# Performance work log

Hardware: AMD Instinct MI355X
Metric: run time of the kernel (lower is better)

The kernel has to match this reference:

```python
import jax, jax.numpy as jnp
import numpy as np

PAD_IDX = 0
NEG = -1e9


def gru_step(h, x, Wih, Whh, bih, bhh):
    # PyTorch GRU cell. Wih: [3H, In], Whh: [3H, H]
    gi = x @ Wih.T + bih
    gh = h @ Whh.T + bhh
    H = h.shape[-1]
    i_r, i_z, i_n = gi[..., :H], gi[..., H:2 * H], gi[..., 2 * H:]
    h_r, h_z, h_n = gh[..., :H], gh[..., H:2 * H], gh[..., 2 * H:]
    r = jax.nn.sigmoid(i_r + h_r)
    z = jax.nn.sigmoid(i_z + h_z)
    n = jnp.tanh(i_n + r * h_n)
    return (1.0 - z) * n + z * h


def setup_inputs() -> dict:
    key = jax.random.key(0)
    V, E, H, C = 256, 512, 1024, 128
    NM, NT, NP = 8, 12, 8
    B, S, T = 256, 96, 40
    ks = iter(jax.random.split(key, 40))

    def p(shape, scale=0.05):
        return (jax.random.normal(next(ks), shape, dtype=jnp.float32) * scale)

    enc_emb = p((V, E)).at[PAD_IDX].set(0.0)
    dec_emb = p((V, E)).at[PAD_IDX].set(0.0)
    inp = dict(
        src=jax.random.randint(next(ks), (B, S), 0, V, dtype=jnp.int32),
        tgt=jax.random.randint(next(ks), (B, T), 0, V, dtype=jnp.int32),
        mode_idx=jax.random.randint(next(ks), (B,), 0, NM, dtype=jnp.int32),
        tense_idx=jax.random.randint(next(ks), (B,), 0, NT, dtype=jnp.int32),
        person_idx=jax.random.randint(next(ks), (B,), 0, NP, dtype=jnp.int32),
        enc_emb=enc_emb,
        enc_Wih_f=p((3 * H, E)), enc_Whh_f=p((3 * H, H)),
        enc_bih_f=p((3 * H,)), enc_bhh_f=p((3 * H,)),
        enc_Wih_b=p((3 * H, E)), enc_Whh_b=p((3 * H, H)),
        enc_bih_b=p((3 * H,)), enc_bhh_b=p((3 * H,)),
        Wa=p((H, 3 * H)),           # attn: Linear(2H + H -> H), no bias
        va=p((1, H)),               # v: Linear(H -> 1), no bias
        dec_emb=dec_emb,
        dec_Wih=p((3 * H, E + 2 * H)), dec_Whh=p((3 * H, H)),
        dec_bih=p((3 * H,)), dec_bhh=p((3 * H,)),
        Wfc=p((V, H + 2 * H + E)), bfc=p((V,)),
        mode_E=p((NM, C)).at[0].set(0.0),
        tense_E=p((NT, C)).at[0].set(0.0),
        person_E=p((NP, C)).at[0].set(0.0),
        Wbr=p((H, 2 * H + 3 * C)), bbr=p((H,)),
    )
    return inp


def reference(src, tgt, mode_idx, tense_idx, person_idx,
              enc_emb, enc_Wih_f, enc_Whh_f, enc_bih_f, enc_bhh_f,
              enc_Wih_b, enc_Whh_b, enc_bih_b, enc_bhh_b,
              Wa, va, dec_emb, dec_Wih, dec_Whh, dec_bih, dec_bhh,
              Wfc, bfc, mode_E, tense_E, person_E, Wbr, bbr):
    B, S = src.shape
    T = tgt.shape[1]
    H = dec_Whh.shape[1]

    # ---- Encoder: bidirectional GRU ----
    x = enc_emb[src]                       # [B,S,E]
    xs = jnp.swapaxes(x, 0, 1)             # [S,B,E]
    h0 = jnp.zeros((B, H), dtype=x.dtype)

    def fstep(h, xt):
        h2 = gru_step(h, xt, enc_Wih_f, enc_Whh_f, enc_bih_f, enc_bhh_f)
        return h2, h2

    def bstep(h, xt):
        h2 = gru_step(h, xt, enc_Wih_b, enc_Whh_b, enc_bih_b, enc_bhh_b)
        return h2, h2

    hf, outs_f = jax.lax.scan(fstep, h0, xs)
    hb, outs_b = jax.lax.scan(bstep, h0, xs[::-1])
    outs_b = outs_b[::-1]
    enc_out = jnp.swapaxes(jnp.concatenate([outs_f, outs_b], axis=-1), 0, 1)  # [B,S,2H]
    enc_hidden = jnp.concatenate([hf, hb], axis=-1)                           # [B,2H]

    # ---- Bridge init of decoder hidden ----
    cond = jnp.concatenate([enc_hidden, mode_E[mode_idx], tense_E[tense_idx],
                            person_E[person_idx]], axis=-1)
    dec_h0 = jnp.tanh(cond @ Wbr.T + bbr)  # [B,H]

    # ---- Attention precompute (linear is separable over the concat) ----
    Wa_h, Wa_e = Wa[:, :H], Wa[:, H:]
    enc_proj = jnp.einsum('bsd,hd->bsh', enc_out, Wa_e)  # [B,S,H]
    src_mask = (src != PAD_IDX)

    # ---- Decoder greedy loop (eval: no teacher forcing) ----
    def step(carry, _):
        h, tok = carry
        energy = jnp.tanh(h @ Wa_h.T[None] if False else jnp.tanh(0))  # placeholder
        energy = jnp.tanh((h @ Wa_h.T)[:, None, :] + enc_proj)          # [B,S,H]
        scores = jnp.einsum('bsh,h->bs', energy, va[0])
        scores = jnp.where(src_mask, scores, NEG)
        w = jax.nn.softmax(scores, axis=-1)
        ctx = jnp.einsum('bs,bsd->bd', w, enc_out)                      # [B,2H]
        emb = dec_emb[tok]                                              # [B,E]
        rnn_in = jnp.concatenate([emb, ctx], axis=-1)
        h2 = gru_step(h, rnn_in, dec_Wih, dec_Whh, dec_bih, dec_bhh)
        pred = jnp.concatenate([h2, ctx, emb], axis=-1) @ Wfc.T + bfc   # [B,V]
        tok2 = jnp.argmax(pred, axis=-1).astype(tok.dtype)
        return (h2, tok2), pred

    (_, _), preds = jax.lax.scan(step, (dec_h0, tgt[:, 0]), None, length=T - 1)
    return jnp.swapaxes(preds, 0, 1)  # [B, T-1, V]
```

## Files before the change

kernel.cpp:

```cpp
#include <hip/hip_runtime.h>
#include <hip/hip_fp16.h>
#include <cstdint>
#include <cstddef>

#define B_  256
#define S_  96
#define T_  40
#define V_  256
#define E_  512
#define H_  1024
#define C_  128

typedef __attribute__((ext_vector_type(8))) short s8v;
typedef __attribute__((ext_vector_type(4))) float f4v;

__device__ __forceinline__ float sigmoidf_(float x) { return 1.0f / (1.0f + expf(-x)); }

__device__ __forceinline__ uint32_t cvtpk_bf16(float a, float b) {
  uint32_t r;
  asm("v_cvt_pk_bf16_f32 %0, %1, %2" : "=v"(r) : "v"(a), "v"(b));
  return r;
}

union U4 { uint32_t u[4]; s8v v; };

__device__ __forceinline__ void split8(const float4 a, const float4 b, s8v& hi, s8v& lo) {
  U4 H, L;
  H.u[0] = cvtpk_bf16(a.x, a.y);
  H.u[1] = cvtpk_bf16(a.z, a.w);
  H.u[2] = cvtpk_bf16(b.x, b.y);
  H.u[3] = cvtpk_bf16(b.z, b.w);
  const float r0 = a.x - __uint_as_float(H.u[0] << 16);
  const float r1 = a.y - __uint_as_float(H.u[0] & 0xffff0000u);
  const float r2 = a.z - __uint_as_float(H.u[1] << 16);
  const float r3 = a.w - __uint_as_float(H.u[1] & 0xffff0000u);
  const float r4 = b.x - __uint_as_float(H.u[2] << 16);
  const float r5 = b.y - __uint_as_float(H.u[2] & 0xffff0000u);
  const float r6 = b.z - __uint_as_float(H.u[3] << 16);
  const float r7 = b.w - __uint_as_float(H.u[3] & 0xffff0000u);
  L.u[0] = cvtpk_bf16(r0, r1);
  L.u[1] = cvtpk_bf16(r2, r3);
  L.u[2] = cvtpk_bf16(r4, r5);
  L.u[3] = cvtpk_bf16(r6, r7);
  hi = H.v; lo = L.v;
}

__global__ void wsplit_k(const float* __restrict__ Wf, const float* __restrict__ Wb,
                         short* __restrict__ hi, short* __restrict__ lo, int n)
{
  const int i = blockIdx.x * 256 + threadIdx.x;
  const float w = (i < n) ? Wf[i] : Wb[i - n];
  const uint32_t h = cvtpk_bf16(w, w) & 0xffffu;
  const float wh = __uint_as_float(h << 16);
  const uint32_t l = cvtpk_bf16(w - wh, w - wh) & 0xffffu;
  hi[i] = (short)h;
  lo[i] = (short)l;
}

__global__ void split_plane_k(const float* __restrict__ src, int ld_src, int col0,
                              short* __restrict__ hi, short* __restrict__ lo,
                              int ld_p, int pcol0, int total, int cols)
{
  const int i = blockIdx.x * 256 + threadIdx.x;
  if (i >= total) return;
  const int r = i / cols, c = i % cols;
  const float w = src[(size_t)r * ld_src + col0 + c];
  const uint32_t h = cvtpk_bf16(w, w) & 0xffffu;
  const float wh = __uint_as_float(h << 16);
  const uint32_t l = cvtpk_bf16(w - wh, w - wh) & 0xffffu;
  const size_t o = (size_t)r * ld_p + pcol0 + c;
  hi[o] = (short)h;
  lo[o] = (short)l;
}

struct EM {
  const int* gidx; int goff0, goff1;
  const float* Gt0; const float* Gt1;
  const float* h0; const float* h1; int ldh;
  const short* whi; const short* wlo;
  const float* bih0; const float* bih1;
  const float* bhh0; const float* bhh1;
  float* d0; float* d1;
  __half* e0; __half* e1; int lde;
};

__global__ __launch_bounds__(256)
void enc_mfma_k(EM g)
{
  const int fid = (blockIdx.x & 7) * 64 + (blockIdx.x >> 3);
  const int m0 = (fid & 3) * 64;
  const int r2 = fid >> 2;
  const int dir = r2 & 1;
  const int q0 = (r2 >> 1) * 16;

  __shared__ int rows[64];
  const int tid = threadIdx.x;
  if (tid < 64)
    rows[tid] = g.gidx[(size_t)(m0 + tid) * S_ + (dir ? g.goff1 : g.goff0)];
  __syncthreads();

  const int w = tid >> 6, lane = tid & 63;
  const int arow = m0 + 16 * w + (lane & 15);
  const int kc = (lane >> 4) << 3;
  const float* hsrc = dir ? g.h1 : g.h0;
  const short* whi = g.whi + (size_t)dir * (3u * H_ * H_);
  const short* wlo = g.wlo + (size_t)dir * (3u * H_ * H_);
  const float* ap = hsrc + (size_t)arow * g.ldh;
  const int wrow = q0 + (lane & 15);

  f4v acc[3];
  acc[0] = f4v{0.f, 0.f, 0.f, 0.f};
  acc[1] = f4v{0.f, 0.f, 0.f, 0.f};
  acc[2] = f4v{0.f, 0.f, 0.f, 0.f};

  float4 a0 = *(const float4*)(ap + kc);
  float4 a1 = *(const float4*)(ap + kc + 4);
  s8v bh[3], bl[3];
#pragma unroll
  for (int g3 = 0; g3 < 3; ++g3) {
    const size_t wb = (size_t)(g3 * H_ + wrow) * H_ + kc;
    bh[g3] = *(const s8v*)(whi + wb);
    bl[g3] = *(const s8v*)(wlo + wb);
  }

  for (int kb = 0; kb < 1024; kb += 32) {
    float4 na0, na1;
    s8v nbh[3], nbl[3];
    if (kb + 32 < 1024) {
      na0 = *(const float4*)(ap + kb + 32 + kc);
      na1 = *(const float4*)(ap + kb + 32 + kc + 4);
#pragma unroll
      for (int g3 = 0; g3 < 3; ++g3) {
        const size_t wb = (size_t)(g3 * H_ + wrow) * H_ + kb + 32 + kc;
        nbh[g3] = *(const s8v*)(whi + wb);
        nbl[g3] = *(const s8v*)(wlo + wb);
      }
    }
    s8v ah, al;
    split8(a0, a1, ah, al);
#pragma unroll
    for (int g3 = 0; g3 < 3; ++g3) {
      acc[g3] = __builtin_amdgcn_mfma_f32_16x16x32_bf16(ah, bh[g3], acc[g3], 0, 0, 0);
      acc[g3] = __builtin_amdgcn_mfma_f32_16x16x32_bf16(al, bh[g3], acc[g3], 0, 0, 0);
      acc[g3] = __builtin_amdgcn_mfma_f32_16x16x32_bf16(ah, bl[g3], acc[g3], 0, 0, 0);
    }
    a0 = na0; a1 = na1;
#pragma unroll
    for (int g3 = 0; g3 < 3; ++g3) { bh[g3] = nbh[g3]; bl[g3] = nbl[g3]; }
  }

  const float* bih = dir ? g.bih1 : g.bih0;
  const float* bhh = dir ? g.bhh1 : g.bhh0;
  const float* Gt = dir ? g.Gt1 : g.Gt0;
  float* dst = dir ? g.d1 : g.d0;
  __half* edst = dir ? g.e1 : g.e0;
  const int col = q0 + (lane & 15);
  const float bir = bih[col], biz = bih[H_ + col], bin = bih[2 * H_ + col];
  const float bhr = bhh[col], bhz = bhh[H_ + col], bhn = bhh[2 * H_ + col];
#pragma unroll
  for (int r = 0; r < 4; ++r) {
    const int b = m0 + 16 * w + (lane >> 4) * 4 + r;
    const float* Gr = Gt + (size_t)rows[b - m0] * (3 * H_);
    const float hold = hsrc[(size_t)b * g.ldh + col];
    const float rr = sigmoidf_(acc[0][r] + Gr[col] + bir + bhr);
    const float zz = sigmoidf_(acc[1][r] + Gr[H_ + col] + biz + bhz);
    const float nn = tanhf(Gr[2 * H_ + col] + bin + rr * (acc[2][r] + bhn));
    const float hv = (1.f - zz) * nn + zz * hold;
    dst[(size_t)b * H_ + col] = hv;
    edst[(size_t)b * g.lde + col] = __float2half(hv);
  }
}

struct DM {
  const float* predin;
  const float* h;
  const int* tok;
  const float* Gd;
  const short* whi; const short* wlo;
  const float* bih; const float* bhh;
  float* d;
  float* predout;
};

__global__ __launch_bounds__(256)
void dec_mfma_k(DM g)
{
  const int fid = (blockIdx.x & 7) * 32 + (blockIdx.x >> 3);
  const int m0 = (fid & 3) * 64;
  const int q0 = (fid >> 2) * 16;
  const int tid = threadIdx.x;
  const int w = tid >> 6, lane = tid & 63;
  const int arow = m0 + 16 * w + (lane & 15);
  const int kc = (lane >> 4) << 3;
  const float* actx = g.predin + (size_t)arow * 3584 + 1024;
  const float* ahid = g.h + (size_t)arow * H_;
  const int wrow = q0 + (lane & 15);

  f4v aR = f4v{0.f,0.f,0.f,0.f}, aZ = aR, aNI = aR, aNH = aR;

  auto loadA = [&](int kk, float4& x0, float4& x1) {
    const float* p = (kk < 2048) ? (actx + kk) : (ahid + kk - 2048);
    x0 = *(const float4*)p;
    x1 = *(const float4*)(p + 4);
  };

  float4 a0, a1;
  loadA(kc, a0, a1);
  s8v bh[3], bl[3];
#pragma unroll
  for (int g3 = 0; g3 < 3; ++g3) {
    const size_t wb = (size_t)(g3 * H_ + wrow) * 3072 + kc;
    bh[g3] = *(const s8v*)(g.whi + wb);
    bl[g3] = *(const s8v*)(g.wlo + wb);
  }

  for (int kb = 0; kb < 3072; kb += 32) {
    float4 na0, na1;
    s8v nbh[3], nbl[3];
    if (kb + 32 < 3072) {
      loadA(kb + 32 + kc, na0, na1);
#pragma unroll
      for (int g3 = 0; g3 < 3; ++g3) {
        const size_t wb = (size_t)(g3 * H_ + wrow) * 3072 + kb + 32 + kc;
        nbh[g3] = *(const s8v*)(g.whi + wb);
        nbl[g3] = *(const s8v*)(g.wlo + wb);
      }
    }
    s8v ah, al;
    split8(a0, a1, ah, al);
    aR = __builtin_amdgcn_mfma_f32_16x16x32_bf16(ah, bh[0], aR, 0, 0, 0);
    aR = __builtin_amdgcn_mfma_f32_16x16x32_bf16(al, bh[0], aR, 0, 0, 0);
    aR = __builtin_amdgcn_mfma_f32_16x16x32_bf16(ah, bl[0], aR, 0, 0, 0);
    aZ = __builtin_amdgcn_mfma_f32_16x16x32_bf16(ah, bh[1], aZ, 0, 0, 0);
    aZ = __builtin_amdgcn_mfma_f32_16x16x32_bf16(al, bh[1], aZ, 0, 0, 0);
    aZ = __builtin_amdgcn_mfma_f32_16x16x32_bf16(ah, bl[1], aZ, 0, 0, 0);
    if (kb < 2048) {
      aNI = __builtin_amdgcn_mfma_f32_16x16x32_bf16(ah, bh[2], aNI, 0, 0, 0);
      aNI = __builtin_amdgcn_mfma_f32_16x16x32_bf16(al, bh[2], aNI, 0, 0, 0);
      aNI = __builtin_amdgcn_mfma_f32_16x16x32_bf16(ah, bl[2], aNI, 0, 0, 0);
    } else {
      aNH = __builtin_amdgcn_mfma_f32_16x16x32_bf16(ah, bh[2], aNH, 0, 0, 0);
      aNH = __builtin_amdgcn_mfma_f32_16x16x32_bf16(al, bh[2], aNH, 0, 0, 0);
      aNH = __builtin_amdgcn_mfma_f32_16x16x32_bf16(ah, bl[2], aNH, 0, 0, 0);
    }
    a0 = na0; a1 = na1;
#pragma unroll
    for (int g3 = 0; g3 < 3; ++g3) { bh[g3] = nbh[g3]; bl[g3] = nbl[g3]; }
  }

  const int col = q0 + (lane & 15);
  const float bir = g.bih[col], biz = g.bih[H_ + col], bin = g.bih[2 * H_ + col];
  const float bhr = g.bhh[col], bhz = g.bhh[H_ + col], bhn = g.bhh[2 * H_ + col];
#pragma unroll
  for (int r = 0; r < 4; ++r) {
    const int b = m0 + 16 * w + (lane >> 4) * 4 + r;
    const float* Gr = g.Gd + (size_t)g.tok[b] * (3 * H_);
    const float hold = g.h[(size_t)b * H_ + col];
    const float rr = sigmoidf_(aR[r] + Gr[col] + bir + bhr);
    const float zz = sigmoidf_(aZ[r] + Gr[H_ + col] + biz + bhz);
    const float nn = tanhf(aNI[r] + Gr[2 * H_ + col] + bin + rr * (aNH[r] + bhn));
    const float hv = (1.f - zz) * nn + zz * hold;
    g.d[(size_t)b * H_ + col] = hv;
    g.predout[(size_t)b * 3584 + col] = hv;
  }
}

__global__ __launch_bounds__(256)
void prqa_mfma_k(const float* __restrict__ predin,
                 const short* __restrict__ fhi, const short* __restrict__ flo,
                 const float* __restrict__ bfc,
                 const float* __restrict__ hnew,
                 const short* __restrict__ qhi, const short* __restrict__ qlo,
                 float* __restrict__ out_t, float* __restrict__ qout)
{
  const int bid = blockIdx.x, tid = threadIdx.x;
  const int w = tid >> 6, lane = tid & 63;
  const int kc = (lane >> 4) << 3;
  if (bid < 256) {
    const int m0 = (bid >> 4) << 4, n0 = (bid & 15) << 4;
    const float* ap = predin + (size_t)(m0 + (lane & 15)) * 3584 + w * 896;
    const short* bhp = fhi + (size_t)(n0 + (lane & 15)) * 3584 + w * 896;
    const short* blp = flo + (size_t)(n0 + (lane & 15)) * 3584 + w * 896;
    f4v acc = f4v{0.f, 0.f, 0.f, 0.f};
    float4 a0 = *(const float4*)(ap + kc), a1 = *(const float4*)(ap + kc + 4);
    s8v bh = *(const s8v*)(bhp + kc), bl = *(const s8v*)(blp + kc);
    for (int kb = 0; kb < 896; kb += 32) {
      float4 na0, na1; s8v nbh, nbl;
      if (kb + 32 < 896) {
        na0 = *(const float4*)(ap + kb + 32 + kc);
        na1 = *(const float4*)(ap + kb + 32 + kc + 4);
        nbh = *(const s8v*)(bhp + kb + 32 + kc);
        nbl = *(const s8v*)(blp + kb + 32 + kc);
      }
      s8v ah, al;
      split8(a0, a1, ah, al);
      acc = __builtin_amdgcn_mfma_f32_16x16x32_bf16(ah, bh, acc, 0, 0, 0);
      acc = __builtin_amdgcn_mfma_f32_16x16x32_bf16(al, bh, acc, 0, 0, 0);
      acc = __builtin_amdgcn_mfma_f32_16x16x32_bf16(ah, bl, acc, 0, 0, 0);
      a0 = na0; a1 = na1; bh = nbh; bl = nbl;
    }
    __shared__ float red[4][64][4];
#pragma unroll
    for (int r = 0; r < 4; ++r) red[w][lane][r] = acc[r];
    __syncthreads();
    const int row = tid >> 4, col = tid & 15;
    const int sl = col + ((row >> 2) << 4), reg = row & 3;
    const float s = red[0][sl][reg] + red[1][sl][reg] + red[2][sl][reg] + red[3][sl][reg];
    out_t[(size_t)(m0 + row) * ((T_ - 1) * V_) + n0 + col] = s + bfc[n0 + col];
  } else {
    const int tt = (bid - 256) * 4 + w;
    const int m0 = (tt >> 6) << 4, n0 = (tt & 63) << 4;
    const float* ap = hnew + (size_t)(m0 + (lane & 15)) * H_;
    const short* bhp = qhi + (size_t)(n0 + (lane & 15)) * H_;
    const short* blp = qlo + (size_t)(n0 + (lane & 15)) * H_;
    f4v acc = f4v{0.f, 0.f, 0.f, 0.f};
    float4 a0 = *(const float4*)(ap + kc), a1 = *(const float4*)(ap + kc + 4);
    s8v bh = *(const s8v*)(bhp + kc), bl = *(const s8v*)(blp + kc);
    for (int kb = 0; kb < 1024; kb += 32) {
      float4 na0, na1; s8v nbh, nbl;
      if (kb + 32 < 1024) {
        na0 = *(const float4*)(ap + kb + 32 + kc);
        na1 = *(const float4*)(ap + kb + 32 + kc + 4);
        nbh = *(const s8v*)(bhp + kb + 32 + kc);
        nbl = *(const s8v*)(blp + kb + 32 + kc);
      }
      s8v ah, al;
      split8(a0, a1, ah, al);
      acc = __builtin_amdgcn_mfma_f32_16x16x32_bf16(ah, bh, acc, 0, 0, 0);
      acc = __builtin_amdgcn_mfma_f32_16x16x32_bf16(al, bh, acc, 0, 0, 0);
      acc = __builtin_amdgcn_mfma_f32_16x16x32_bf16(ah, bl, acc, 0, 0, 0);
      a0 = na0; a1 = na1; bh = nbh; bl = nbl;
    }
#pragma unroll
    for (int r = 0; r < 4; ++r)
      qout[(size_t)(m0 + (lane >> 4) * 4 + r) * H_ + n0 + (lane & 15)] = acc[r];
  }
}

__global__ __launch_bounds__(512)
void attn1_k(const float* __restrict__ out, const int* __restrict__ tgt,
             const float* __restrict__ q, const __half* __restrict__ proj,
             const float* __restrict__ va, const int* __restrict__ src,
             const float* __restrict__ dec_emb,
             float* __restrict__ predin, float* __restrict__ wts,
             int* __restrict__ tokbuf, int t)
{
  const int b = blockIdx.x, tid = threadIdx.x;
  const int lane = tid & 63, wv = tid >> 6;
  __shared__ float sm[128];
  __shared__ float tr[128];
  __shared__ float rv[4];
  __shared__ int ri[4];
  __shared__ int tok_s;
  if (t == 0) {
    if (tid == 0) tok_s = tgt[(size_t)b * T_];
  } else {
    if (tid < 256) {
      float av = out[((size_t)b * (T_ - 1) + (t - 1)) * V_ + tid];
      int ai = tid;
      for (int off = 32; off; off >>= 1) {
        const float ov = __shfl_down(av, off);
        const int   oi = __shfl_down(ai, off);
        if (ov > av) { av = ov; ai = oi; }
      }
      if (lane == 0) { rv[wv] = av; ri[wv] = ai; }
    }
    __syncthreads();
    if (tid == 0) {
      float bv = rv[0]; int bi = ri[0];
      for (int w2 = 1; w2 < 4; ++w2) if (rv[w2] > bv) { bv = rv[w2]; bi = ri[w2]; }
      tok_s = bi;
    }
  }
  __syncthreads();
  const int tok = tok_s;
  if (tid == 0) tokbuf[b] = tok;
  predin[(size_t)b * 3584 + 3072 + tid] = dec_emb[(size_t)tok * E_ + tid];
  const float* qb = q + (size_t)b * H_;
  for (int s = wv * 12; s < wv * 12 + 12; ++s) {
    const __half* pb = proj + ((size_t)b * S_ + s) * H_;
    float part = 0.f;
#pragma unroll
    for (int j = 0; j < 8; ++j) {
      const int h = lane * 2 + j * 128;
      const __half2 p2 = *(const __half2*)(pb + h);
      const float2 q2 = *(const float2*)(qb + h);
      const float2 v2 = *(const float2*)(va + h);
      part += v2.x * tanhf(q2.x + __half2float(p2.x));
      part += v2.y * tanhf(q2.y + __half2float(p2.y));
    }
    for (int off = 32; off; off >>= 1) part += __shfl_down(part, off);
    if (lane == 0)
      sm[s] = (src[(size_t)b * S_ + s] == 0) ? -1.0e9f : part;
  }
  __syncthreads();
  if (tid < 128) tr[tid] = (tid < S_) ? sm[tid] : -3.0e38f;
  __syncthreads();
  for (int s2 = 64; s2 > 0; s2 >>= 1) { if (tid < s2) tr[tid] = fmaxf(tr[tid], tr[tid + s2]); __syncthreads(); }
  const float mx = tr[0];
  __syncthreads();
  if (tid < 128) tr[tid] = (tid < S_) ? expf(sm[tid] - mx) : 0.f;
  __syncthreads();
  for (int s2 = 64; s2 > 0; s2 >>= 1) { if (tid < s2) tr[tid] += tr[tid + s2]; __syncthreads(); }
  const float inv = 1.0f / tr[0];
  __syncthreads();
  if (tid < S_) wts[(size_t)b * S_ + tid] = expf(sm[tid] - mx) * inv;
}

__global__ __launch_bounds__(256)
void ctx_k(const float* __restrict__ wts, const __half* __restrict__ enc,
           float* __restrict__ predin)
{
  const int b = blockIdx.y, tid = threadIdx.x;
  __shared__ float sw[S_];
  if (tid < S_) sw[tid] = wts[(size_t)b * S_ + tid];
  __syncthreads();
  const int d = blockIdx.x * 512 + tid * 2;
  const __half* eb = enc + (size_t)b * S_ * (2 * H_) + d;
  float c0 = 0.f, c1 = 0.f;
  for (int s0 = 0; s0 < S_; s0 += 8) {
    __half2 v[8];
#pragma unroll
    for (int i = 0; i < 8; ++i) v[i] = *(const __half2*)(eb + (size_t)(s0 + i) * (2 * H_));
#pragma unroll
    for (int i = 0; i < 8; ++i) {
      const float w = sw[s0 + i];
      c0 += w * __half2float(v[i].x);
      c1 += w * __half2float(v[i].y);
    }
  }
  *(float2*)(predin + (size_t)b * 3584 + H_ + d) = make_float2(c0, c1);
}

struct GB {
  const float* A; int lda;
  const __half* Ah;
  const float* W; int ldw;
  const float* bias;
  float* C; int ldc;
  __half* Ch;
  int M, N, K, act;
  const float *hf, *hb; int ldh;
  const float *mE, *tE, *pE;
  const int *mi, *ti, *pi;
};

template<int AMODE, int CMODE>
__global__ __launch_bounds__(256)
void gemm_k(GB g0, GB g1)
{
  GB g = blockIdx.z ? g1 : g0;
  const int m0 = blockIdx.y * 64, n0 = blockIdx.x * 64;
  if (m0 >= g.M || n0 >= g.N) return;
  __shared__ float As[32][68];
  __shared__ float Ws[32][68];
  const int tid = threadIdx.x, tx = tid & 15, ty = tid >> 4;
  const int lm = tid >> 3, lk = (tid & 7) << 2;
  float acc[4][4] = {};
  float4 av[2], wv[2], av2[2], wv2[2];

  auto load_tile = [&](int k0, float4 (&AV)[2], float4 (&WV)[2]) {
#pragma unroll
    for (int i = 0; i < 2; ++i) {
      const int row = lm + i * 32;
      const int kk = k0 + lk;
      if (AMODE == 0) {
        AV[i] = *(const float4*)(g.A + (size_t)(m0 + row) * g.lda + kk);
      } else if (AMODE == 4) {
        const __half* ap = g.Ah + (size_t)(m0 + row) * g.lda + kk;
        const __half2 h0 = *(const __half2*)ap;
        const __half2 h1 = *(const __half2*)(ap + 2);
        AV[i] = make_float4(__half2float(h0.x), __half2float(h0.y),
                            __half2float(h1.x), __half2float(h1.y));
      } else {
        const int mg = m0 + row; const float* sp; size_t o;
        if (kk < 1024)      { sp = g.hf; o = (size_t)mg * g.ldh + kk; }
        else if (kk < 2048) { sp = g.hb; o = (size_t)mg * g.ldh + kk - 1024; }
        else if (kk < 2176) { sp = g.mE; o = (size_t)g.mi[mg] * C_ + kk - 2048; }
        else if (kk < 2304) { sp = g.tE; o = (size_t)g.ti[mg] * C_ + kk - 2176; }
        else                { sp = g.pE; o = (size_t)g.pi[mg] * C_ + kk - 2304; }
        AV[i] = *(const float4*)(sp + o);
      }
      WV[i] = *(const float4*)(g.W + (size_t)(n0 + row) * g.ldw + kk);
    }
  };

  load_tile(0, av, wv);
  for (int k0 = 0; k0 < g.K; k0 += 32) {
    __syncthreads();
#pragma unroll
    for (int i = 0; i < 2; ++i) {
      const int row = lm + i * 32;
      As[lk + 0][row] = av[i].x; As[lk + 1][row] = av[i].y;
      As[lk + 2][row] = av[i].z; As[lk + 3][row] = av[i].w;
      Ws[lk + 0][row] = wv[i].x; Ws[lk + 1][row] = wv[i].y;
      Ws[lk + 2][row] = wv[i].z; Ws[lk + 3][row] = wv[i].w;
    }
    __syncthreads();
    if (k0 + 32 < g.K) load_tile(k0 + 32, av2, wv2);
#pragma unroll
    for (int k = 0; k < 32; ++k) {
      const float4 a4 = *(const float4*)&As[k][ty << 2];
      const float4 b4 = *(const float4*)&Ws[k][tx << 2];
      acc[0][0] += a4.x * b4.x; acc[0][1] += a4.x * b4.y; acc[0][2] += a4.x * b4.z; acc[0][3] += a4.x * b4.w;
      acc[1][0] += a4.y * b4.x; acc[1][1] += a4.y * b4.y; acc[1][2] += a4.y * b4.z; acc[1][3] += a4.y * b4.w;
      acc[2][0] += a4.z * b4.x; acc[2][1] += a4.z * b4.y; acc[2][2] += a4.z * b4.z; acc[2][3] += a4.z * b4.w;
      acc[3][0] += a4.w * b4.x; acc[3][1] += a4.w * b4.y; acc[3][2] += a4.w * b4.z; acc[3][3] += a4.w * b4.w;
    }
#pragma unroll
    for (int i = 0; i < 2; ++i) { av[i] = av2[i]; wv[i] = wv2[i]; }
  }
  const int n = n0 + (tx << 2);
  float4 bb = make_float4(0.f, 0.f, 0.f, 0.f);
  if (g.bias) bb = *(const float4*)(g.bias + n);
#pragma unroll
  for (int i = 0; i < 4; ++i) {
    const int m = m0 + (ty << 2) + i;
    float4 v = make_float4(acc[i][0] + bb.x, acc[i][1] + bb.y, acc[i][2] + bb.z, acc[i][3] + bb.w);
    if (CMODE == 0) {
      if (g.act) { v.x = tanhf(v.x); v.y = tanhf(v.y); v.z = tanhf(v.z); v.w = tanhf(v.w); }
      *(float4*)(g.C + (size_t)m * g.ldc + n) = v;
    } else {
      __half2* cp = (__half2*)(g.Ch + (size_t)m * g.ldc + n);
      cp[0] = __floats2half2_rn(v.x, v.y);
      cp[1] = __floats2half2_rn(v.z, v.w);
    }
  }
}

__global__ void zero_k(float* __restrict__ p, int n)
{
  const int i = blockIdx.x * 256 + threadIdx.x;
  if (i < n) p[i] = 0.0f;
}

__global__ void sentinel_k(float* out, float v) { out[threadIdx.x] = v; }

extern "C" void kernel_launch(void* const* d_in, const int* in_sizes, int n_in,
                              void* d_out, int out_size, void* d_ws, size_t ws_size,
                              hipStream_t stream)
{
  const int*   src        = (const int*)d_in[0];
  const int*   tgt        = (const int*)d_in[1];
  const int*   mode_idx   = (const int*)d_in[2];
  const int*   tense_idx  = (const int*)d_in[3];
  const int*   person_idx = (const int*)d_in[4];
  const float* enc_emb    = (const float*)d_in[5];
  const float* eWih_f     = (const float*)d_in[6];
  const float* eWhh_f     = (const float*)d_in[7];
  const float* ebih_f     = (const float*)d_in[8];
  const float* ebhh_f     = (const float*)d_in[9];
  const float* eWih_b     = (const float*)d_in[10];
  const float* eWhh_b     = (const float*)d_in[11];
  const float* ebih_b     = (const float*)d_in[12];
  const float* ebhh_b     = (const float*)d_in[13];
  const float* Wa         = (const float*)d_in[14];
  const float* va         = (const float*)d_in[15];
  const float* dec_emb    = (const float*)d_in[16];
  const float* dWih       = (const float*)d_in[17];
  const float* dWhh       = (const float*)d_in[18];
  const float* dbih       = (const float*)d_in[19];
  const float* dbhh       = (const float*)d_in[20];
  const float* Wfc        = (const float*)d_in[21];
  const float* bfc        = (const float*)d_in[22];
  const float* mode_E     = (const float*)d_in[23];
  const float* tense_E    = (const float*)d_in[24];
  const float* person_E   = (const float*)d_in[25];
  const float* Wbr        = (const float*)d_in[26];
  const float* bbr        = (const float*)d_in[27];
  float* out = (float*)d_out;

  char* base = (char*)d_ws;
  size_t off = 0;
  auto alloc = [&](size_t bytes) { char* r = base + off; off = (off + bytes + 255) & ~(size_t)255; return r; };
  __half* enc_out = (__half*)alloc(2ull * B_ * S_ * 2 * H_);
  __half* proj    = (__half*)alloc(2ull * B_ * S_ * H_);
  short* whh_hi = (short*)alloc(2ull * 2 * 3 * H_ * H_);
  short* whh_lo = (short*)alloc(2ull * 2 * 3 * H_ * H_);
  short* dpl_hi = (short*)alloc(2ull * 3 * H_ * 3072);
  short* dpl_lo = (short*)alloc(2ull * 3 * H_ * 3072);
  short* fc_hi  = (short*)alloc(2ull * V_ * 3584);
  short* fc_lo  = (short*)alloc(2ull * V_ * 3584);
  short* qa_hi  = (short*)alloc(2ull * H_ * H_);
  short* qa_lo  = (short*)alloc(2ull * H_ * H_);
  float* Gi_f  = (float*)alloc(4ull * V_ * 3 * H_);
  float* Gi_b  = (float*)alloc(4ull * V_ * 3 * H_);
  float* Gd    = (float*)alloc(4ull * V_ * 3 * H_);
  float* hfA   = (float*)alloc(4ull * B_ * H_);
  float* hfB   = (float*)alloc(4ull * B_ * H_);
  float* hbA   = (float*)alloc(4ull * B_ * H_);
  float* hbB   = (float*)alloc(4ull * B_ * H_);
  float* h_d0  = (float*)alloc(4ull * B_ * H_);
  float* h_d1  = (float*)alloc(4ull * B_ * H_);
  float* q     = (float*)alloc(4ull * B_ * H_);
  float* predin = (float*)alloc(4ull * B_ * 3584);
  float* wts   = (float*)alloc(4ull * B_ * S_);
  int*   tok   = (int*)alloc(4ull * B_);
  float* zero_buf = (float*)alloc(4ull * 1024);
  if (off > ws_size) {
    hipLaunchKernelGGL(sentinel_k, dim3(1), dim3(256), 0, stream, out,
                       1000.0f + (float)(ws_size >> 20));
    return;
  }

  hipLaunchKernelGGL(zero_k, dim3(4), dim3(256), 0, stream, zero_buf, 1024);

  {
    const int n = 3 * H_ * H_;
    hipLaunchKernelGGL(wsplit_k, dim3((2 * n) / 256), dim3(256), 0, stream,
                       eWhh_f, eWhh_b, whh_hi, whh_lo, n);
    int tot = 3 * H_ * 2048;
    hipLaunchKernelGGL(split_plane_k, dim3((tot + 255) / 256), dim3(256), 0, stream,
                       dWih, 2560, 512, dpl_hi, dpl_lo, 3072, 0, tot, 2048);
    tot = 3 * H_ * 1024;
    hipLaunchKernelGGL(split_plane_k, dim3((tot + 255) / 256), dim3(256), 0, stream,
                       dWhh, 1024, 0, dpl_hi, dpl_lo, 3072, 2048, tot, 1024);
    tot = V_ * 3584;
    hipLaunchKernelGGL(split_plane_k, dim3((tot + 255) / 256), dim3(256), 0, stream,
                       Wfc, 3584, 0, fc_hi, fc_lo, 3584, 0, tot, 3584);
    tot = H_ * 1024;
    hipLaunchKernelGGL(split_plane_k, dim3((tot + 255) / 256), dim3(256), 0, stream,
                       Wa, 3 * H_, 0, qa_hi, qa_lo, 1024, 0, tot, 1024);
  }

  GB Z{};

  {
    GB t0 = Z, t1 = Z;
    t0.A = enc_emb; t0.lda = E_; t0.W = eWih_f; t0.ldw = E_;
    t0.C = Gi_f; t0.ldc = 3 * H_; t0.M = V_; t0.N = 3 * H_; t0.K = E_;
    t1 = t0; t1.W = eWih_b; t1.C = Gi_b;
    hipLaunchKernelGGL((gemm_k<0, 0>), dim3(48, 4, 2), dim3(256), 0, stream, t0, t1);
    GB t2 = Z;
    t2.A = dec_emb; t2.lda = E_; t2.W = dWih; t2.ldw = 2560;
    t2.C = Gd; t2.ldc = 3 * H_; t2.M = V_; t2.N = 3 * H_; t2.K = E_;
    hipLaunchKernelGGL((gemm_k<0, 0>), dim3(48, 4, 1), dim3(256), 0, stream, t2, t2);
  }

  for (int t = 0; t < S_; ++t) {
    EM em{};
    em.gidx = src; em.goff0 = t; em.goff1 = S_ - 1 - t;
    em.Gt0 = Gi_f; em.Gt1 = Gi_b;
    if (t == 0) { em.h0 = zero_buf; em.h1 = zero_buf; em.ldh = 0; }
    else if (t & 1) { em.h0 = hfA; em.h1 = hbA; em.ldh = H_; }
    else            { em.h0 = hfB; em.h1 = hbB; em.ldh = H_; }
    em.whi = whh_hi; em.wlo = whh_lo;
    em.bih0 = ebih_f; em.bih1 = ebih_b; em.bhh0 = ebhh_f; em.bhh1 = ebhh_b;
    if (t & 1) { em.d0 = hfB; em.d1 = hbB; } else { em.d0 = hfA; em.d1 = hbA; }
    em.e0 = enc_out + (size_t)t * 2 * H_;
    em.e1 = enc_out + (size_t)(S_ - 1 - t) * 2 * H_ + H_;
    em.lde = S_ * 2 * H_;
    hipLaunchKernelGGL(enc_mfma_k, dim3(512), dim3(256), 0, stream, em);
  }
  float* hf_fin = hfB;
  float* hb_fin = hbB;

  {
    GB ep = Z;
    ep.Ah = enc_out; ep.lda = 2 * H_; ep.W = Wa + H_; ep.ldw = 3 * H_;
    ep.Ch = proj; ep.ldc = H_; ep.M = B_ * S_; ep.N = H_; ep.K = 2 * H_;
    hipLaunchKernelGGL((gemm_k<4, 1>), dim3(16, 384, 1), dim3(256), 0, stream, ep, ep);
  }

  {
    GB br = Z;
    br.W = Wbr; br.ldw = 2432; br.bias = bbr; br.C = h_d0; br.ldc = H_;
    br.M = B_; br.N = H_; br.K = 2432; br.act = 1;
    br.hf = hf_fin; br.hb = hb_fin; br.ldh = H_;
    br.mE = mode_E; br.tE = tense_E; br.pE = person_E;
    br.mi = mode_idx; br.ti = tense_idx; br.pi = person_idx;
    hipLaunchKernelGGL((gemm_k<2, 0>), dim3(16, 4, 1), dim3(256), 0, stream, br, br);
  }

  {
    GB qa = Z;
    qa.A = h_d0; qa.lda = H_; qa.W = Wa; qa.ldw = 3 * H_; qa.C = q; qa.ldc = H_;
    qa.M = B_; qa.N = H_; qa.K = H_;
    hipLaunchKernelGGL((gemm_k<0, 0>), dim3(16, 4, 1), dim3(256), 0, stream, qa, qa);
  }

  float* hd[2] = { h_d0, h_d1 };
  for (int t = 0; t < T_ - 1; ++t) {
    hipLaunchKernelGGL(attn1_k, dim3(B_), dim3(512), 0, stream,
                       out, tgt, q, proj, va, src, dec_emb, predin, wts, tok, t);
    hipLaunchKernelGGL(ctx_k, dim3(4, B_), dim3(256), 0, stream, wts, enc_out, predin);

    DM dm{};
    dm.predin = predin;
    dm.h = hd[t & 1];
    dm.tok = tok; dm.Gd = Gd;
    dm.whi = dpl_hi; dm.wlo = dpl_lo;
    dm.bih = dbih; dm.bhh = dbhh;
    dm.d = hd[(t + 1) & 1];
    dm.predout = predin;
    hipLaunchKernelGGL(dec_mfma_k, dim3(256), dim3(256), 0, stream, dm);

    hipLaunchKernelGGL(prqa_mfma_k, dim3(512), dim3(256), 0, stream,
                       predin, fc_hi, fc_lo, bfc, hd[(t + 1) & 1], qa_hi, qa_lo,
                       out + (size_t)t * V_, q);
  }
}
```

Measured before the change: 14.94 ms.

## Split decoder GRU gates across waves and add MFMA kernel for attention projection

The decoder GRU kernel now runs 12 waves per block, one gate per group of four waves, instead of 4 waves each handling all three gates. The split bf16 activation tile is staged in double-buffered shared memory so it is converted once and reused by every gate. Gate results are then combined through shared memory. Separately, the one-off encoder projection GEMM is moved from the generic gemm_k path to a dedicated fp16 MFMA kernel, using a hi/lo split of the Wa_e weights and 2 MFMAs per step. The aim is more parallelism per decoder step and tensor-core use for the projection, at the cost of a __syncthreads per K chunk and a different precision scheme for the projection.

After: 14.27 ms (median of 2 runs). -4.5%, faster.

```diff
diff --git a/kernel.cpp b/kernel.cpp
--- a/kernel.cpp
+++ b/kernel.cpp
@@ -13,6 +13,7 @@
 
 typedef __attribute__((ext_vector_type(8))) short s8v;
 typedef __attribute__((ext_vector_type(4))) float f4v;
+typedef _Float16 h8v __attribute__((ext_vector_type(8)));
 
 __device__ __forceinline__ float sigmoidf_(float x) { return 1.0f / (1.0f + expf(-x)); }
 
@@ -73,6 +74,21 @@
   lo[o] = (short)l;
 }
 
+__global__ void split_plane_h_k(const float* __restrict__ src, int ld_src, int col0,
+                                __half* __restrict__ hi, __half* __restrict__ lo,
+                                int ld_p, int total, int cols)
+{
+  const int i = blockIdx.x * 256 + threadIdx.x;
+  if (i >= total) return;
+  const int r = i / cols, c = i % cols;
+  const float w = src[(size_t)r * ld_src + col0 + c];
+  const __half h = __float2half(w);
+  const __half l = __float2half(w - __half2float(h));
+  const size_t o = (size_t)r * ld_p + c;
+  hi[o] = h;
+  lo[o] = l;
+}
+
 struct EM {
   const int* gidx; int goff0, goff1;
   const float* Gt0; const float* Gt1;
@@ -182,7 +198,7 @@
   float* predout;
 };
 
-__global__ __launch_bounds__(256)
+__global__ __launch_bounds__(768)
 void dec_mfma_k(DM g)
 {
   const int fid = (blockIdx.x & 7) * 32 + (blockIdx.x >> 3);
@@ -190,79 +206,158 @@
   const int q0 = (fid >> 2) * 16;
   const int tid = threadIdx.x;
   const int w = tid >> 6, lane = tid & 63;
-  const int arow = m0 + 16 * w + (lane & 15);
-  const int kc = (lane >> 4) << 3;
-  const float* actx = g.predin + (size_t)arow * 3584 + 1024;
-  const float* ahid = g.h + (size_t)arow * H_;
-  const int wrow = q0 + (lane & 15);
-
-  f4v aR = f4v{0.f,0.f,0.f,0.f}, aZ = aR, aNI = aR, aNH = aR;
-
-  auto loadA = [&](int kk, float4& x0, float4& x1) {
+  const int mg = w & 3;
+  const int gate = w >> 2;
+
+  __shared__ short sA[2][2][64][40];
+  __shared__ float eacc[4][64][16];
+
+  const int srow = tid >> 2;
+  const int skq = (tid & 3) << 3;
+  const float* actx = g.predin + (size_t)(m0 + srow) * 3584 + 1024;
+  const float* ahid = g.h + (size_t)(m0 + srow) * H_;
+  auto loadA8 = [&](int kk, float4& x0, float4& x1) {
     const float* p = (kk < 2048) ? (actx + kk) : (ahid + kk - 2048);
     x0 = *(const float4*)p;
     x1 = *(const float4*)(p + 4);
   };
 
-  float4 a0, a1;
-  loadA(kc, a0, a1);
-  s8v bh[3], bl[3];
-#pragma unroll
-  for (int g3 = 0; g3 < 3; ++g3) {
-    const size_t wb = (size_t)(g3 * H_ + wrow) * 3072 + kc;
-    bh[g3] = *(const s8v*)(g.whi + wb);
-    bl[g3] = *(const s8v*)(g.wlo + wb);
-  }
-
-  for (int kb = 0; kb < 3072; kb += 32) {
-    float4 na0, na1;
-    s8v nbh[3], nbl[3];
-    if (kb + 32 < 3072) {
-      loadA(kb + 32 + kc, na0, na1);
-#pragma unroll
-      for (int g3 = 0; g3 < 3; ++g3) {
-        const size_t wb = (size_t)(g3 * H_ + wrow) * 3072 + kb + 32 + kc;
-        nbh[g3] = *(const s8v*)(g.whi + wb);
-        nbl[g3] = *(const s8v*)(g.wlo + wb);
-      }
-    }
+  const int kc = (lane >> 4) << 3;
+  const int wrow = gate * H_ + q0 + (lane & 15);
+  const short* whp = g.whi + (size_t)wrow * 3072 + kc;
+  const short* wlp = g.wlo + (size_t)wrow * 3072 + kc;
+
+  f4v acc0 = f4v{0.f, 0.f, 0.f, 0.f};
+  f4v acc1 = acc0;
+
+  float4 sx0, sx1;
+  if (tid < 256) loadA8(skq, sx0, sx1);
+  s8v bh = *(const s8v*)whp;
+  s8v bl = *(const s8v*)wlp;
+  if (tid < 256) {
     s8v ah, al;
-    split8(a0, a1, ah, al);
-    aR = __builtin_amdgcn_mfma_f32_16x16x32_bf16(ah, bh[0], aR, 0, 0, 0);
-    aR = __builtin_amdgcn_mfma_f32_16x16x32_bf16(al, bh[0], aR, 0, 0, 0);
-    aR = __builtin_amdgcn_mfma_f32_16x16x32_bf16(ah, bl[0], aR, 0, 0, 0);
-    aZ = __builtin_amdgcn_mfma_f32_16x16x32_bf16(ah, bh[1], aZ, 0, 0, 0);
-    aZ = __builtin_amdgcn_mfma_f32_16x16x32_bf16(al, bh[1], aZ, 0, 0, 0);
-    aZ = __builtin_amdgcn_mfma_f32_16x16x32_bf16(ah, bl[1], aZ, 0, 0, 0);
-    if (kb < 2048) {
-      aNI = __builtin_amdgcn_mfma_f32_16x16x32_bf16(ah, bh[2], aNI, 0, 0, 0);
-      aNI = __builtin_amdgcn_mfma_f32_16x16x32_bf16(al, bh[2], aNI, 0, 0, 0);
-      aNI = __builtin_amdgcn_mfma_f32_16x16x32_bf16(ah, bl[2], aNI, 0, 0, 0);
+    split8(sx0, sx1, ah, al);
+    *(s8v*)&sA[0][0][srow][skq] = ah;
+    *(s8v*)&sA[0][1][srow][skq] = al;
+  }
+  __syncthreads();
+
+  const int arowl = mg * 16 + (lane & 15);
+  for (int ch = 0; ch < 96; ++ch) {
+    const int buf = ch & 1;
+    float4 nx0, nx1;
+    if (tid < 256 && ch + 1 < 96) loadA8((ch + 1) * 32 + skq, nx0, nx1);
+    s8v nbh, nbl;
+    if (ch + 1 < 96) {
+      nbh = *(const s8v*)(whp + (ch + 1) * 32);
+      nbl = *(const s8v*)(wlp + (ch + 1) * 32);
+    }
+    const s8v ah = *(const s8v*)&sA[buf][0][arowl][kc];
+    const s8v al = *(const s8v*)&sA[buf][1][arowl][kc];
+    if (gate < 2) {
+      acc0 = __builtin_amdgcn_mfma_f32_16x16x32_bf16(ah, bh, acc0, 0, 0, 0);
+      acc0 = __builtin_amdgcn_mfma_f32_16x16x32_bf16(al, bh, acc0, 0, 0, 0);
+      acc0 = __builtin_amdgcn_mfma_f32_16x16x32_bf16(ah, bl, acc0, 0, 0, 0);
+    } else if (ch < 64) {
+      acc0 = __builtin_amdgcn_mfma_f32_16x16x32_bf16(ah, bh, acc0, 0, 0, 0);
+      acc0 = __builtin_amdgcn_mfma_f32_16x16x32_bf16(al, bh, acc0, 0, 0, 0);
+      acc0 = __builtin_amdgcn_mfma_f32_16x16x32_bf16(ah, bl, acc0, 0, 0, 0);
     } else {
-      aNH = __builtin_amdgcn_mfma_f32_16x16x32_bf16(ah, bh[2], aNH, 0, 0, 0);
-      aNH = __builtin_amdgcn_mfma_f32_16x16x32_bf16(al, bh[2], aNH, 0, 0, 0);
-      aNH = __builtin_amdgcn_mfma_f32_16x16x32_bf16(ah, bl[2], aNH, 0, 0, 0);
-    }
-    a0 = na0; a1 = na1;
-#pragma unroll
-    for (int g3 = 0; g3 < 3; ++g3) { bh[g3] = nbh[g3]; bl[g3] = nbl[g3]; }
-  }
-
-  const int col = q0 + (lane & 15);
-  const float bir = g.bih[col], biz = g.bih[H_ + col], bin = g.bih[2 * H_ + col];
-  const float bhr = g.bhh[col], bhz = g.bhh[H_ + col], bhn = g.bhh[2 * H_ + col];
+      acc1 = __builtin_amdgcn_mfma_f32_16x16x32_bf16(ah, bh, acc1, 0, 0, 0);
+      acc1 = __builtin_amdgcn_mfma_f32_16x16x32_bf16(al, bh, acc1, 0, 0, 0);
+      acc1 = __builtin_amdgcn_mfma_f32_16x16x32_bf16(ah, bl, acc1, 0, 0, 0);
+    }
+    if (tid < 256 && ch + 1 < 96) {
+      s8v ah2, al2;
+      split8(nx0, nx1, ah2, al2);
+      *(s8v*)&sA[buf ^ 1][0][srow][skq] = ah2;
+      *(s8v*)&sA[buf ^ 1][1][srow][skq] = al2;
+    }
+    bh = nbh; bl = nbl;
+    __syncthreads();
+  }
+
 #pragma unroll
   for (int r = 0; r < 4; ++r) {
-    const int b = m0 + 16 * w + (lane >> 4) * 4 + r;
+    const int lr = mg * 16 + (lane >> 4) * 4 + r;
+    if (gate < 2) {
+      eacc[gate][lr][lane & 15] = acc0[r];
+    } else {
+      eacc[2][lr][lane & 15] = acc0[r];
+      eacc[3][lr][lane & 15] = acc1[r];
+    }
+  }
+  __syncthreads();
+
+  for (int o = tid; o < 1024; o += 768) {
+    const int lr = o >> 4, lc = o & 15;
+    const int b = m0 + lr, col = q0 + lc;
     const float* Gr = g.Gd + (size_t)g.tok[b] * (3 * H_);
     const float hold = g.h[(size_t)b * H_ + col];
-    const float rr = sigmoidf_(aR[r] + Gr[col] + bir + bhr);
-    const float zz = sigmoidf_(aZ[r] + Gr[H_ + col] + biz + bhz);
-    const float nn = tanhf(aNI[r] + Gr[2 * H_ + col] + bin + rr * (aNH[r] + bhn));
+    const float rr = sigmoidf_(eacc[0][lr][lc] + Gr[col] + g.bih[col] + g.bhh[col]);
+    const float zz = sigmoidf_(eacc[1][lr][lc] + Gr[H_ + col] + g.bih[H_ + col] + g.bhh[H_ + col]);
+    const float nn = tanhf(eacc[2][lr][lc] + Gr[2 * H_ + col] + g.bih[2 * H_ + col]
+                           + rr * (eacc[3][lr][lc] + g.bhh[2 * H_ + col]));
     const float hv = (1.f - zz) * nn + zz * hold;
     g.d[(size_t)b * H_ + col] = hv;
     g.predout[(size_t)b * 3584 + col] = hv;
   }
+}
+
+__global__ __launch_bounds__(256)
+void proj_mfma_k(const __half* __restrict__ enc, const __half* __restrict__ whi,
+                 const __half* __restrict__ wlo, __half* __restrict__ proj)
+{
+  const int fid = (blockIdx.x & 7) * 768 + (blockIdx.x >> 3);
+  const int w = threadIdx.x >> 6, lane = threadIdx.x & 63;
+  const int wg = fid * 4 + w;
+  const int ng = wg / 1536;
+  const int mt = wg % 1536;
+  const int n0 = ng * 64;
+  const int kc = (lane >> 4) << 3;
+  const __half* ap = enc + (size_t)(mt * 16 + (lane & 15)) * 2048 + kc;
+  const __half* bhp = whi + (size_t)(n0 + (lane & 15)) * 2048 + kc;
+  const __half* blp = wlo + (size_t)(n0 + (lane & 15)) * 2048 + kc;
+
+  f4v acc[4];
+#pragma unroll
+  for (int j = 0; j < 4; ++j) acc[j] = f4v{0.f, 0.f, 0.f, 0.f};
+
+  h8v a = *(const h8v*)ap;
+  h8v bh[4], bl[4];
+#pragma unroll
+  for (int j = 0; j < 4; ++j) {
+    bh[j] = *(const h8v*)(bhp + (size_t)j * 16 * 2048);
+    bl[j] = *(const h8v*)(blp + (size_t)j * 16 * 2048);
+  }
+
+  for (int kb = 0; kb < 2048; kb += 32) {
+    h8v na, nbh[4], nbl[4];
+    if (kb + 32 < 2048) {
+      na = *(const h8v*)(ap + kb + 32);
+#pragma unroll
+      for (int j = 0; j < 4; ++j) {
+        nbh[j] = *(const h8v*)(bhp + (size_t)j * 16 * 2048 + kb + 32);
+        nbl[j] = *(const h8v*)(blp + (size_t)j * 16 * 2048 + kb + 32);
+      }
+    }
+#pragma unroll
+    for (int j = 0; j < 4; ++j) {
+      acc[j] = __builtin_amdgcn_mfma_f32_16x16x32_f16(a, bh[j], acc[j], 0, 0, 0);
+      acc[j] = __builtin_amdgcn_mfma_f32_16x16x32_f16(a, bl[j], acc[j], 0, 0, 0);
+    }
+    a = na;
+#pragma unroll
+    for (int j = 0; j < 4; ++j) { bh[j] = nbh[j]; bl[j] = nbl[j]; }
+  }
+
+#pragma unroll
+  for (int j = 0; j < 4; ++j)
+#pragma unroll
+    for (int r = 0; r < 4; ++r) {
+      const int row = mt * 16 + (lane >> 4) * 4 + r;
+      proj[(size_t)row * H_ + n0 + j * 16 + (lane & 15)] = __float2half(acc[j][r]);
+    }
 }
 
 __global__ __launch_bounds__(256)
@@ -583,6 +678,8 @@
   short* fc_lo  = (short*)alloc(2ull * V_ * 3584);
   short* qa_hi  = (short*)alloc(2ull * H_ * H_);
   short* qa_lo  = (short*)alloc(2ull * H_ * H_);
+  __half* wae_hi = (__half*)alloc(2ull * H_ * 2048);
+  __half* wae_lo = (__half*)alloc(2ull * H_ * 2048);
   float* Gi_f  = (float*)alloc(4ull * V_ * 3 * H_);
   float* Gi_b  = (float*)alloc(4ull * V_ * 3 * H_);
   float* Gd    = (float*)alloc(4ull * V_ * 3 * H_);
@@ -621,6 +718,9 @@
     tot = H_ * 1024;
     hipLaunchKernelGGL(split_plane_k, dim3((tot + 255) / 256), dim3(256), 0, stream,
                        Wa, 3 * H_, 0, qa_hi, qa_lo, 1024, 0, tot, 1024);
+    tot = H_ * 2048;
+    hipLaunchKernelGGL(split_plane_h_k, dim3((tot + 255) / 256), dim3(256), 0, stream,
+                       Wa, 3 * H_, 1024, wae_hi, wae_lo, 2048, tot, 2048);
   }
 
   GB Z{};
@@ -655,12 +755,8 @@
   float* hf_fin = hfB;
   float* hb_fin = hbB;
 
-  {
-    GB ep = Z;
-    ep.Ah = enc_out; ep.lda = 2 * H_; ep.W = Wa + H_; ep.ldw = 3 * H_;
-    ep.Ch = proj; ep.ldc = H_; ep.M = B_ * S_; ep.N = H_; ep.K = 2 * H_;
-    hipLaunchKernelGGL((gemm_k<4, 1>), dim3(16, 384, 1), dim3(256), 0, stream, ep, ep);
-  }
+  hipLaunchKernelGGL(proj_mfma_k, dim3(6144), dim3(256), 0, stream,
+                     enc_out, wae_hi, wae_lo, proj);
 
   {
     GB br = Z;
@@ -693,7 +789,7 @@
     dm.bih = dbih; dm.bhh = dbhh;
     dm.d = hd[(t + 1) & 1];
     dm.predout = predin;
-    hipLaunchKernelGGL(dec_mfma_k, dim3(256), dim3(256), 0, stream, dm);
+    hipLaunchKernelGGL(dec_mfma_k, dim3(256), dim3(768), 0, stream, dm);
 
     hipLaunchKernelGGL(prqa_mfma_k, dim3(512), dim3(256), 0, stream,
                        predin, fc_hi, fc_lo, bfc, hd[(t + 1) & 1], qa_hi, qa_lo,
```
